# Performance work log

Hardware: AMD Instinct MI355X
Metric: run time of the kernel (lower is better)

Reference implementation:

```python
import jax, jax.numpy as jnp
import numpy as np

H = 1024           # hidden_size
NH = 16            # num_attention_heads
HD = H // NH       # attention_head_size
MAX_POS = 1024
LN_EPS = 1e-12


def setup_inputs() -> dict:
    key = jax.random.key(0)
    ks = jax.random.split(key, 10)
    s = 0.02
    return {
        "hidden_states": jax.random.normal(ks[0], (8, 1024, H), dtype=jnp.float32),
        "pos_emb": jax.random.normal(ks[1], (MAX_POS, H), dtype=jnp.float32) * s,
        "ln_w": jnp.ones((H,), dtype=jnp.float32),
        "ln_b": jnp.zeros((H,), dtype=jnp.float32),
        "wq": jax.random.normal(ks[2], (H, H), dtype=jnp.float32) * s,
        "bq": jnp.zeros((H,), dtype=jnp.float32),
        "wk": jax.random.normal(ks[3], (H, H), dtype=jnp.float32) * s,
        "bk": jnp.zeros((H,), dtype=jnp.float32),
        "wv": jax.random.normal(ks[4], (H, H), dtype=jnp.float32) * s,
        "bv": jnp.zeros((H,), dtype=jnp.float32),
    }


def _split_heads(x):
    # [B, S, H] -> [B, NH, S, HD]
    b, s, _ = x.shape
    return x.reshape(b, s, NH, HD).transpose(0, 2, 1, 3)


def reference(hidden_states, pos_emb, ln_w, ln_b, wq, bq, wk, bk, wv, bv):
    b, s, h = hidden_states.shape
    # add position embeddings for positions [0, s)
    x = hidden_states + pos_emb[:s][None, :, :]
    # LayerNorm
    mu = jnp.mean(x, axis=-1, keepdims=True)
    var = jnp.mean(jnp.square(x - mu), axis=-1, keepdims=True)
    x = (x - mu) * jax.lax.rsqrt(var + LN_EPS) * ln_w + ln_b
    # QKV projections (torch Linear: y = x @ W^T + b)
    q = _split_heads(x @ wq.T + bq)   # [B, NH, S, HD]
    k = _split_heads(x @ wk.T + bk)
    v = _split_heads(x @ wv.T + bv)
    # scaled dot-product attention, full score matrix (as in original)
    scores = jnp.einsum("bnqd,bnkd->bnqk", q, k) / jnp.sqrt(jnp.float32(HD))
    probs = jax.nn.softmax(scores, axis=-1)
    ctx = jnp.einsum("bnqk,bnkd->bnqd", probs, v)  # [B, NH, S, HD]
    ctx = ctx.transpose(0, 2, 1, 3).reshape(b, s, h)
    return ctx
```

## Files before the change

kernel.cpp:

```cpp
#include <hip/hip_runtime.h>
#include <stdint.h>

typedef short short8 __attribute__((ext_vector_type(8)));
typedef short s16x4 __attribute__((ext_vector_type(4)));
typedef float f32x4 __attribute__((ext_vector_type(4)));

#define NB_H  1024
#define NB_NH 16
#define NB_HD 64
#define NB_B  8
#define NB_S  1024

__device__ __forceinline__ unsigned short f2bf(float f) {
    union { float f; unsigned u; } v; v.f = f;
    unsigned u = v.u;
    return (unsigned short)((u + 0x7fffu + ((u >> 16) & 1u)) >> 16);
}

__device__ __forceinline__ float exp2_fast(float x) {
    float r; asm("v_exp_f32 %0, %1" : "=v"(r) : "v"(x)); return r;
}

__device__ __forceinline__ void gload16(const void* g, void* l) {
    __builtin_amdgcn_global_load_lds(
        (const __attribute__((address_space(1))) void*)g,
        (__attribute__((address_space(3))) void*)l,
        16, 0, 0);
}

__global__ __launch_bounds__(256) void prologue_kernel(
    const float* __restrict__ wq, const float* __restrict__ wk, const float* __restrict__ wv,
    short* __restrict__ wbf,
    const float* __restrict__ hs, const float* __restrict__ pos,
    const float* __restrict__ lnw, const float* __restrict__ lnb,
    short* __restrict__ xbf)
{
    const int t = threadIdx.x;
    if (blockIdx.x < 3072) {
        unsigned i = (blockIdx.x * 256u + t) * 4u;
        const float* src = (i < (1u << 20)) ? wq : (i < (2u << 20)) ? wk : wv;
        const float4 v = *(const float4*)(src + (i & 0xFFFFFu));
        s16x4 o;
        o[0] = (short)f2bf(v.x); o[1] = (short)f2bf(v.y);
        o[2] = (short)f2bf(v.z); o[3] = (short)f2bf(v.w);
        *(s16x4*)(wbf + i) = o;
        return;
    }
    const int row = blockIdx.x - 3072;
    const int s   = row & 1023;
    const int wave = t >> 6, lane = t & 63;

    float4 x4 = *(const float4*)(hs  + (size_t)row * 1024 + t * 4);
    float4 p4 = *(const float4*)(pos + (size_t)s   * 1024 + t * 4);
    float v0 = x4.x + p4.x, v1 = x4.y + p4.y, v2 = x4.z + p4.z, v3 = x4.w + p4.w;

    float sum = v0 + v1 + v2 + v3;
    #pragma unroll
    for (int o = 1; o < 64; o <<= 1) sum += __shfl_xor(sum, o, 64);
    __shared__ float red[4];
    __shared__ float red2[4];
    if (lane == 0) red[wave] = sum;
    __syncthreads();
    float mu = (red[0] + red[1] + red[2] + red[3]) * (1.0f / 1024.0f);

    float d0 = v0 - mu, d1 = v1 - mu, d2 = v2 - mu, d3 = v3 - mu;
    float sq = d0 * d0 + d1 * d1 + d2 * d2 + d3 * d3;
    #pragma unroll
    for (int o = 1; o < 64; o <<= 1) sq += __shfl_xor(sq, o, 64);
    if (lane == 0) red2[wave] = sq;
    __syncthreads();
    float var = (red2[0] + red2[1] + red2[2] + red2[3]) * (1.0f / 1024.0f);
    float rs = rsqrtf(var + 1e-12f);

    const float4 w4 = *(const float4*)(lnw + t * 4);
    const float4 b4 = *(const float4*)(lnb + t * 4);
    s16x4 o;
    o[0] = (short)f2bf(d0 * rs * w4.x + b4.x);
    o[1] = (short)f2bf(d1 * rs * w4.y + b4.y);
    o[2] = (short)f2bf(d2 * rs * w4.z + b4.z);
    o[3] = (short)f2bf(d3 * rs * w4.w + b4.w);
    *(s16x4*)(xbf + (size_t)row * 1024 + t * 4) = o;
}

__global__ __launch_bounds__(256, 4) void qkv_gemm(
    const short* __restrict__ xbf,
    const short* __restrict__ wbf,
    const float* __restrict__ bq, const float* __restrict__ bk, const float* __restrict__ bv,
    short* __restrict__ q_bf, short* __restrict__ k_bf, short* __restrict__ vt_bf)
{
    __shared__ short lds_a[128 * 64];
    __shared__ short lds_b[128 * 64];

    const int tid = threadIdx.x;
    const int wave = tid >> 6, lane = tid & 63;
    const int l15 = lane & 15, l4 = lane >> 4;
    const int m0 = blockIdx.x * 128;
    const int n0 = blockIdx.y * 128;
    const int wr = wave >> 1, wc = wave & 1;

    f32x4 acc[4][4] = {};

    const short* pA[4];
    const short* pB[4];
    short* ldsA[4];
    short* ldsB[4];
    #pragma unroll
    for (int i = 0; i < 4; ++i) {
        const int chunk = i * 256 + tid;
        const int srow = chunk >> 3;
        const int scol = (chunk & 7) ^ (srow & 7);
        pA[i] = xbf + (size_t)(m0 + srow) * 1024 + scol * 8;
        pB[i] = wbf + (size_t)(n0 + srow) * 1024 + scol * 8;
        ldsA[i] = lds_a + chunk * 8;
        ldsB[i] = lds_b + chunk * 8;
    }

    int offA[2][4], offB[2][4];
    #pragma unroll
    for (int ks = 0; ks < 2; ++ks) {
        #pragma unroll
        for (int mi = 0; mi < 4; ++mi) {
            const int ar = wr * 64 + mi * 16 + l15;
            offA[ks][mi] = ar * 64 + (((ks * 4 + l4) ^ (ar & 7)) << 3);
            const int br = wc * 64 + mi * 16 + l15;
            offB[ks][mi] = br * 64 + (((ks * 4 + l4) ^ (br & 7)) << 3);
        }
    }

    #pragma unroll 1
    for (int kt = 0; kt < 16; ++kt) {
        __syncthreads();
        #pragma unroll
        for (int i = 0; i < 4; ++i) {
            gload16(pA[i], ldsA[i]);
            gload16(pB[i], ldsB[i]);
            pA[i] += 64;
            pB[i] += 64;
        }
        __syncthreads();
        #pragma unroll
        for (int ks = 0; ks < 2; ++ks) {
            short8 af[4], bfr[4];
            #pragma unroll
            for (int mi = 0; mi < 4; ++mi) af[mi] = *(const short8*)(lds_a + offA[ks][mi]);
            #pragma unroll
            for (int nj = 0; nj < 4; ++nj) bfr[nj] = *(const short8*)(lds_b + offB[ks][nj]);
            __builtin_amdgcn_s_setprio(1);
            #pragma unroll
            for (int mi = 0; mi < 4; ++mi)
                #pragma unroll
                for (int nj = 0; nj < 4; ++nj)
                    acc[mi][nj] = __builtin_amdgcn_mfma_f32_16x16x32_bf16(af[mi], bfr[nj], acc[mi][nj], 0, 0, 0);
            __builtin_amdgcn_s_setprio(0);
        }
    }

    #pragma unroll
    for (int mi = 0; mi < 4; ++mi)
        #pragma unroll
        for (int nj = 0; nj < 4; ++nj) {
            const int n = n0 + wc * 64 + nj * 16 + l15;
            const int which = n >> 10;
            const int hh = (n >> 6) & 15, dd = n & 63, nn = n & 1023;
            const float bias = (which == 0) ? bq[nn] : (which == 1) ? bk[nn] : bv[nn];
            const int mbase = m0 + wr * 64 + mi * 16 + l4 * 4;
            const int bi = mbase >> 10, s0 = mbase & 1023;
            if (which == 2) {
                s16x4 hv4;
                #pragma unroll
                for (int r = 0; r < 4; ++r) hv4[r] = (short)f2bf(acc[mi][nj][r] + bias);
                *(s16x4*)(vt_bf + (size_t)((bi * 16 + hh) * 64 + dd) * 1024 + s0) = hv4;
            } else {
                #pragma unroll
                for (int r = 0; r < 4; ++r) {
                    float val = acc[mi][nj][r] + bias;
                    if (which == 0) val *= 0.18033688f;
                    const short hv = (short)f2bf(val);
                    if (which == 0) q_bf[(size_t)((bi * 16 + hh) * 1024 + s0 + r) * 64 + dd] = hv;
                    else            k_bf[(size_t)((bi * 16 + hh) * 1024 + s0 + r) * 64 + dd] = hv;
                }
            }
        }
}

__global__ __launch_bounds__(256, 3) void attn_kernel(
    const short* __restrict__ q_bf, const short* __restrict__ k_bf,
    const short* __restrict__ vt_bf, float* __restrict__ out)
{
    __shared__ short lds_k[2][64 * 64];
    __shared__ short lds_v[2][64 * 64];

    const int lin = blockIdx.x;
    const int xcd = lin & 7, kk = lin >> 3;
    const int bh = xcd * 16 + (kk & 15);
    const int qt = kk >> 4;
    const int bi = bh >> 4, hh = bh & 15;
    const int tid = threadIdx.x, wave = tid >> 6, lane = tid & 63;
    const int l15 = lane & 15, l4 = lane >> 4;
    const int qrow0 = qt * 128 + wave * 32;

    const short* qb = q_bf  + (size_t)bh * NB_S * NB_HD;
    const short* kb = k_bf  + (size_t)bh * NB_S * NB_HD;
    const short* vb = vt_bf + (size_t)bh * NB_HD * NB_S;

    short8 qa[2][2];
    #pragma unroll
    for (int mi = 0; mi < 2; ++mi)
        #pragma unroll
        for (int ks = 0; ks < 2; ++ks)
            qa[mi][ks] = *(const short8*)(qb + (size_t)(qrow0 + mi * 16 + l15) * 64 + ks * 32 + l4 * 8);

    f32x4 oacc[2][4] = {};
    float mrun[2], lsum[2];
    mrun[0] = mrun[1] = -1e30f;
    lsum[0] = lsum[1] = 0.0f;

    const short* pK[2];
    const short* pV[2];
    int ldsOff[2];
    #pragma unroll
    for (int c = 0; c < 2; ++c) {
        const int chunk = c * 256 + tid;
        const int row = chunk >> 3;
        const int scc = (chunk & 7) ^ (row & 7);
        pK[c] = kb + (size_t)row * 64 + scc * 8;
        pV[c] = vb + (size_t)row * 1024 + scc * 8;
        ldsOff[c] = chunk * 8;
    }
    auto stage = [&](int sl) {
        #pragma unroll
        for (int c = 0; c < 2; ++c) {
            gload16(pK[c], &lds_k[0][0] + sl * 4096 + ldsOff[c]);
            gload16(pV[c], &lds_v[0][0] + sl * 4096 + ldsOff[c]);
            pK[c] += 4096;
            pV[c] += 64;
        }
    };

    int koff[4][2], voff[4][4];
    #pragma unroll
    for (int kt = 0; kt < 4; ++kt) {
        #pragma unroll
        for (int ks = 0; ks < 2; ++ks) {
            const int r = kt * 16 + l15;
            koff[kt][ks] = r * 64 + (((ks * 4 + l4) ^ (r & 7)) << 3);
        }
        #pragma unroll
        for (int nj = 0; nj < 4; ++nj) {
            const int row = nj * 16 + l15;
            voff[nj][kt] = row * 64 + (((kt * 2 + (l4 >> 1)) ^ (row & 7)) << 3) + (l4 & 1) * 4;
        }
    }

    auto compute = [&](int bt) {
        const short* kbase = &lds_k[0][0] + bt * 4096;
        const short* vbase = &lds_v[0][0] + bt * 4096;

        short8 kf[4][2];
        #pragma unroll
        for (int kt = 0; kt < 4; ++kt)
            #pragma unroll
            for (int ks = 0; ks < 2; ++ks)
                kf[kt][ks] = *(const short8*)(kbase + koff[kt][ks]);

        f32x4 sacc[2][4] = {};
        __builtin_amdgcn_s_setprio(1);
        #pragma unroll
        for (int mi = 0; mi < 2; ++mi)
            #pragma unroll
            for (int kt = 0; kt < 4; ++kt)
                #pragma unroll
                for (int ks = 0; ks < 2; ++ks)
                    sacc[mi][kt] = __builtin_amdgcn_mfma_f32_16x16x32_bf16(kf[kt][ks], qa[mi][ks], sacc[mi][kt], 0, 0, 0);
        __builtin_amdgcn_s_setprio(0);

        s16x4 vf[4][4];
        #pragma unroll
        for (int nj = 0; nj < 4; ++nj)
            #pragma unroll
            for (int kt = 0; kt < 4; ++kt)
                vf[nj][kt] = *(const s16x4*)(vbase + voff[nj][kt]);

        s16x4 pa[2][4];
        #pragma unroll
        for (int mi = 0; mi < 2; ++mi) {
            float a0 = fmaxf(fmaxf(sacc[mi][0][0], sacc[mi][0][1]), fmaxf(sacc[mi][0][2], sacc[mi][0][3]));
            float a1 = fmaxf(fmaxf(sacc[mi][1][0], sacc[mi][1][1]), fmaxf(sacc[mi][1][2], sacc[mi][1][3]));
            float a2 = fmaxf(fmaxf(sacc[mi][2][0], sacc[mi][2][1]), fmaxf(sacc[mi][2][2], sacc[mi][2][3]));
            float a3 = fmaxf(fmaxf(sacc[mi][3][0], sacc[mi][3][1]), fmaxf(sacc[mi][3][2], sacc[mi][3][3]));
            float tm = fmaxf(fmaxf(a0, a1), fmaxf(a2, a3));
            if (!__all(tm <= mrun[mi] + 8.0f)) {
                tm = fmaxf(tm, __shfl_xor(tm, 16, 64));
                tm = fmaxf(tm, __shfl_xor(tm, 32, 64));
                const float mnew = fmaxf(mrun[mi], tm);
                const float fac = exp2_fast(mrun[mi] - mnew);
                lsum[mi] *= fac;
                #pragma unroll
                for (int nj = 0; nj < 4; ++nj)
                    #pragma unroll
                    for (int r = 0; r < 4; ++r) oacc[mi][nj][r] *= fac;
                mrun[mi] = mnew;
            }
            const float mcur = mrun[mi];
            float rsum = 0.0f;
            #pragma unroll
            for (int kt = 0; kt < 4; ++kt) {
                float p0 = exp2_fast(sacc[mi][kt][0] - mcur);
                float p1 = exp2_fast(sacc[mi][kt][1] - mcur);
                float p2 = exp2_fast(sacc[mi][kt][2] - mcur);
                float p3 = exp2_fast(sacc[mi][kt][3] - mcur);
                rsum += (p0 + p1) + (p2 + p3);
                union { s16x4 v; unsigned u[2]; } pu;
                asm("v_cvt_pk_bf16_f32 %0, %1, %2" : "=v"(pu.u[0]) : "v"(p0), "v"(p1));
                asm("v_cvt_pk_bf16_f32 %0, %1, %2" : "=v"(pu.u[1]) : "v"(p2), "v"(p3));
                pa[mi][kt] = pu.v;
            }
            lsum[mi] += rsum;
        }

        __builtin_amdgcn_s_setprio(1);
        #pragma unroll
        for (int nj = 0; nj < 4; ++nj)
            #pragma unroll
            for (int kt = 0; kt < 4; ++kt)
                #pragma unroll
                for (int mi = 0; mi < 2; ++mi)
                    oacc[mi][nj] = __builtin_amdgcn_mfma_f32_16x16x16bf16_1k(
                        vf[nj][kt], pa[mi][kt], oacc[mi][nj], 0, 0, 0);
        __builtin_amdgcn_s_setprio(0);
    };

    stage(0);
    stage(1);

    #pragma unroll 1
    for (int t = 0; t < 14; ++t) {
        asm volatile("s_waitcnt vmcnt(4)" ::: "memory");
        __builtin_amdgcn_s_barrier();
        compute(t & 1);
        __builtin_amdgcn_s_barrier();
        stage(t & 1);
    }
    asm volatile("s_waitcnt vmcnt(4)" ::: "memory");
    __builtin_amdgcn_s_barrier();
    compute(0);
    asm volatile("s_waitcnt vmcnt(0)" ::: "memory");
    __builtin_amdgcn_s_barrier();
    compute(1);

    #pragma unroll
    for (int mi = 0; mi < 2; ++mi) {
        float l = lsum[mi];
        l += __shfl_xor(l, 16, 64);
        l += __shfl_xor(l, 32, 64);
        const float inv = 1.0f / l;
        #pragma unroll
        for (int nj = 0; nj < 4; ++nj) {
            float4 v;
            v.x = oacc[mi][nj][0] * inv;
            v.y = oacc[mi][nj][1] * inv;
            v.z = oacc[mi][nj][2] * inv;
            v.w = oacc[mi][nj][3] * inv;
            *(float4*)(out + ((size_t)bi * 1024 + qrow0 + mi * 16 + l15) * 1024
                           + hh * 64 + nj * 16 + l4 * 4) = v;
        }
    }
}

extern "C" void kernel_launch(void* const* d_in, const int* in_sizes, int n_in,
                              void* d_out, int out_size, void* d_ws, size_t ws_size,
                              hipStream_t stream) {
    const float* hs  = (const float*)d_in[0];
    const float* pos = (const float*)d_in[1];
    const float* lnw = (const float*)d_in[2];
    const float* lnb = (const float*)d_in[3];
    const float* wq  = (const float*)d_in[4];
    const float* bq  = (const float*)d_in[5];
    const float* wk  = (const float*)d_in[6];
    const float* bk  = (const float*)d_in[7];
    const float* wv  = (const float*)d_in[8];
    const float* bv  = (const float*)d_in[9];
    float* out = (float*)d_out;

    char* ws = (char*)d_ws;
    short* wbf  = (short*)(ws);
    short* xbf  = (short*)(ws + 6291456);
    short* qbf  = (short*)(ws + 6291456 + 16777216);
    short* kbf  = (short*)(ws + 6291456 + 2 * 16777216);
    short* vtbf = (short*)(ws + 6291456 + 3 * 16777216);

    prologue_kernel<<<dim3(11264), dim3(256), 0, stream>>>(
        wq, wk, wv, wbf, hs, pos, lnw, lnb, xbf);
    qkv_gemm<<<dim3(64, 24), dim3(256), 0, stream>>>(xbf, wbf, bq, bk, bv, qbf, kbf, vtbf);
    attn_kernel<<<dim3(1024), dim3(256), 0, stream>>>(qbf, kbf, vtbf, out);
}
```

Before: 122.4 us.

## Double-buffer QKV GEMM LDS tiles with async prefetch and vmcnt waits

Splits the QKV GEMM's K tile from 64 to 32 and keeps two LDS buffers, so global-to-LDS loads for the next tile are issued while the MFMAs run on the current one. Partial s_waitcnt vmcnt counts replace the full syncthreads drain. The intent is to hide global load latency behind compute. In exchange there are twice as many barriers per unit of K work and a hand-counted vmcnt that must match the number of outstanding loads.

```diff
diff --git a/kernel.cpp b/kernel.cpp
--- a/kernel.cpp
+++ b/kernel.cpp
@@ -88,8 +88,8 @@
     const float* __restrict__ bq, const float* __restrict__ bk, const float* __restrict__ bv,
     short* __restrict__ q_bf, short* __restrict__ k_bf, short* __restrict__ vt_bf)
 {
-    __shared__ short lds_a[128 * 64];
-    __shared__ short lds_b[128 * 64];
+    __shared__ short lds_a[2][128 * 32];
+    __shared__ short lds_b[2][128 * 32];
 
     const int tid = threadIdx.x;
     const int wave = tid >> 6, lane = tid & 63;
@@ -100,60 +100,69 @@
 
     f32x4 acc[4][4] = {};
 
-    const short* pA[4];
-    const short* pB[4];
-    short* ldsA[4];
-    short* ldsB[4];
-    #pragma unroll
-    for (int i = 0; i < 4; ++i) {
+    const short* pA[2];
+    const short* pB[2];
+    int ldsOff[2];
+    #pragma unroll
+    for (int i = 0; i < 2; ++i) {
         const int chunk = i * 256 + tid;
-        const int srow = chunk >> 3;
-        const int scol = (chunk & 7) ^ (srow & 7);
+        const int srow = chunk >> 2;
+        const int scol = (chunk & 3) ^ (srow & 3);
         pA[i] = xbf + (size_t)(m0 + srow) * 1024 + scol * 8;
         pB[i] = wbf + (size_t)(n0 + srow) * 1024 + scol * 8;
-        ldsA[i] = lds_a + chunk * 8;
-        ldsB[i] = lds_b + chunk * 8;
-    }
-
-    int offA[2][4], offB[2][4];
-    #pragma unroll
-    for (int ks = 0; ks < 2; ++ks) {
-        #pragma unroll
-        for (int mi = 0; mi < 4; ++mi) {
-            const int ar = wr * 64 + mi * 16 + l15;
-            offA[ks][mi] = ar * 64 + (((ks * 4 + l4) ^ (ar & 7)) << 3);
-            const int br = wc * 64 + mi * 16 + l15;
-            offB[ks][mi] = br * 64 + (((ks * 4 + l4) ^ (br & 7)) << 3);
-        }
-    }
+        ldsOff[i] = chunk * 8;
+    }
+    auto stage = [&](int sl) {
+        #pragma unroll
+        for (int i = 0; i < 2; ++i) {
+            gload16(pA[i], &lds_a[sl][ldsOff[i]]);
+            gload16(pB[i], &lds_b[sl][ldsOff[i]]);
+            pA[i] += 32;
+            pB[i] += 32;
+        }
+    };
+
+    int offA[4], offB[4];
+    #pragma unroll
+    for (int mi = 0; mi < 4; ++mi) {
+        const int ar = wr * 64 + mi * 16 + l15;
+        offA[mi] = ar * 32 + ((l4 ^ (ar & 3)) << 3);
+        const int br = wc * 64 + mi * 16 + l15;
+        offB[mi] = br * 32 + ((l4 ^ (br & 3)) << 3);
+    }
+
+    auto compute = [&](int sl) {
+        short8 af[4], bfr[4];
+        #pragma unroll
+        for (int mi = 0; mi < 4; ++mi) af[mi] = *(const short8*)(&lds_a[sl][offA[mi]]);
+        #pragma unroll
+        for (int nj = 0; nj < 4; ++nj) bfr[nj] = *(const short8*)(&lds_b[sl][offB[nj]]);
+        __builtin_amdgcn_s_setprio(1);
+        #pragma unroll
+        for (int mi = 0; mi < 4; ++mi)
+            #pragma unroll
+            for (int nj = 0; nj < 4; ++nj)
+                acc[mi][nj] = __builtin_amdgcn_mfma_f32_16x16x32_bf16(af[mi], bfr[nj], acc[mi][nj], 0, 0, 0);
+        __builtin_amdgcn_s_setprio(0);
+    };
+
+    stage(0);
+    stage(1);
 
     #pragma unroll 1
-    for (int kt = 0; kt < 16; ++kt) {
-        __syncthreads();
-        #pragma unroll
-        for (int i = 0; i < 4; ++i) {
-            gload16(pA[i], ldsA[i]);
-            gload16(pB[i], ldsB[i]);
-            pA[i] += 64;
-            pB[i] += 64;
-        }
-        __syncthreads();
-        #pragma unroll
-        for (int ks = 0; ks < 2; ++ks) {
-            short8 af[4], bfr[4];
-            #pragma unroll
-            for (int mi = 0; mi < 4; ++mi) af[mi] = *(const short8*)(lds_a + offA[ks][mi]);
-            #pragma unroll
-            for (int nj = 0; nj < 4; ++nj) bfr[nj] = *(const short8*)(lds_b + offB[ks][nj]);
-            __builtin_amdgcn_s_setprio(1);
-            #pragma unroll
-            for (int mi = 0; mi < 4; ++mi)
-                #pragma unroll
-                for (int nj = 0; nj < 4; ++nj)
-                    acc[mi][nj] = __builtin_amdgcn_mfma_f32_16x16x32_bf16(af[mi], bfr[nj], acc[mi][nj], 0, 0, 0);
-            __builtin_amdgcn_s_setprio(0);
-        }
-    }
+    for (int kt = 0; kt < 30; ++kt) {
+        asm volatile("s_waitcnt vmcnt(4)" ::: "memory");
+        __builtin_amdgcn_s_barrier();
+        compute(kt & 1);
+        __builtin_amdgcn_s_barrier();
+        stage(kt & 1);
+    }
+    asm volatile("s_waitcnt vmcnt(4)" ::: "memory");
+    __builtin_amdgcn_s_barrier();
+    compute(0);
+    asm volatile("s_waitcnt vmcnt(0)" ::: "memory");
+    __builtin_amdgcn_s_barrier();
+    compute(1);
 
     #pragma unroll
     for (int mi = 0; mi < 4; ++mi)
```

Measured after the change: 134.7 us. 1.1x slower.
